# Performance work log

Hardware: AMD Instinct MI355X
Metric: run time of the kernel (lower is better)

Reference implementation:

```python
import jax, jax.numpy as jnp
import numpy as np


def setup_inputs() -> dict:
    key = jax.random.key(0)
    ks = jax.random.split(key, 4)
    B, H, W, C = 4, 64, 64, 64
    d = C // 8
    s = 0.05
    return {
        "x": jax.random.normal(ks[0], (B, H, W, C), dtype=jnp.float32),
        "Wq": jax.random.normal(ks[1], (C, d), dtype=jnp.float32) * s,
        "bq": jnp.zeros((d,), dtype=jnp.float32),
        "Wk": jax.random.normal(ks[2], (C, d), dtype=jnp.float32) * s,
        "bk": jnp.zeros((d,), dtype=jnp.float32),
        "Wv": jax.random.normal(ks[3], (C, C), dtype=jnp.float32) * s,
        "bv": jnp.zeros((C,), dtype=jnp.float32),
        "gamma": jnp.zeros((1,), dtype=jnp.float32),
    }


def reference(x, Wq, bq, Wk, bk, Wv, bv, gamma):
    B, H, W, C = x.shape
    N = H * W
    xt = x.reshape(B, N, C)  # tokens = flattened spatial positions
    # 1x1 convs == per-token matmuls
    q = xt @ Wq + bq          # [B, N, C//8]
    k = xt @ Wk + bk          # [B, N, C//8]
    v = xt @ Wv + bv          # [B, N, C]
    # unscaled QK^T softmax (SAGAN uses no 1/sqrt(d) scaling)
    attn = jax.nn.softmax(jnp.einsum('bnd,bmd->bnm', q, k), axis=-1)  # [B, N, N]
    out = jnp.einsum('bnm,bmc->bnc', attn, v).reshape(B, H, W, C)
    return gamma * out + x
```

## Files before the change

kernel.cpp:

```cpp
#include <hip/hip_runtime.h>
#include <hip/hip_bf16.h>


typedef __attribute__((ext_vector_type(4))) float f32x4;
typedef __attribute__((ext_vector_type(8))) short short8;

#define LOG2E 1.44269504088896340736f

#if __has_builtin(__builtin_amdgcn_exp2f)
#define EXP2(x) __builtin_amdgcn_exp2f(x)
#else
#define EXP2(x) __builtin_exp2f(x)
#endif

__device__ __forceinline__ unsigned short f2bf(float f) {
    __hip_bfloat16 h = __float2bfloat16(f);
    union { __hip_bfloat16 h; unsigned short u; } cv;
    cv.h = h;
    return cv.u;
}

__device__ __forceinline__ float bf2f(unsigned short u) {
    union { unsigned int i; float f; } cv;
    cv.i = ((unsigned int)u) << 16;
    return cv.f;
}

__global__ __launch_bounds__(256) void sagan_proj_kernel(
    const float* __restrict__ x,
    const float* __restrict__ Wq, const float* __restrict__ bq,
    const float* __restrict__ Wk, const float* __restrict__ bk,
    const float* __restrict__ Wv, const float* __restrict__ bv,
    unsigned short* __restrict__ Qb, unsigned short* __restrict__ Kb,
    unsigned char* __restrict__ V8, unsigned short* __restrict__ zp)
{
    __shared__ float xs[32][68];
    const int tid = threadIdx.x;
    const int blk = blockIdx.x;
    const int tglob0 = blk << 5;
    const int b  = tglob0 >> 12;
    const int nb = tglob0 & 4095;

    if (blk == 0 && tid < 8) zp[tid] = 0;

    {
        const int t = tid >> 3, q8 = tid & 7;
        const float* src = x + (size_t)(tglob0 + t) * 64 + q8 * 8;
        *(f32x4*)&xs[t][q8 * 8]     = *(const f32x4*)(src);
        *(f32x4*)&xs[t][q8 * 8 + 4] = *(const f32x4*)(src + 4);
    }
    __syncthreads();

    {
        const int c  = tid & 63;
        const int tg = tid >> 6;
        float wcol[64];
        #pragma unroll
        for (int cc = 0; cc < 64; ++cc) wcol[cc] = Wv[cc * 64 + c];
        const float bvc = bv[c];
        float vacc[8];
        #pragma unroll
        for (int j = 0; j < 8; ++j) {
            const int tok = tg * 8 + j;
            float acc = bvc;
            #pragma unroll
            for (int c4 = 0; c4 < 16; ++c4) {
                f32x4 xv = *(const f32x4*)&xs[tok][c4 * 4];
                acc += xv[0] * wcol[c4 * 4 + 0] + xv[1] * wcol[c4 * 4 + 1]
                     + xv[2] * wcol[c4 * 4 + 2] + xv[3] * wcol[c4 * 4 + 3];
            }
            vacc[j] = acc;
        }
        int i0 = __builtin_amdgcn_cvt_pk_fp8_f32(vacc[0], vacc[1], 0, false);
        i0     = __builtin_amdgcn_cvt_pk_fp8_f32(vacc[2], vacc[3], i0, true);
        int i1 = __builtin_amdgcn_cvt_pk_fp8_f32(vacc[4], vacc[5], 0, false);
        i1     = __builtin_amdgcn_cvt_pk_fp8_f32(vacc[6], vacc[7], i1, true);
        unsigned char* dst = V8 + ((size_t)((b * 128 + (nb >> 5)) * 64 + c)) * 32
                                + tg * 8;
        *(uint2*)dst = make_uint2((unsigned int)i0, (unsigned int)i1);
    }

    {
        const int tok = tid >> 3;
        const int dd  = tid & 7;
        float q0 = bq[dd];
        float k0 = bk[dd];
        #pragma unroll
        for (int cc = 0; cc < 64; ++cc) {
            const float xv = xs[tok][cc];
            q0 += xv * Wq[cc * 8 + dd];
            k0 += xv * Wk[cc * 8 + dd];
        }
        const size_t toff = (size_t)(tglob0 + tok) * 8 + dd;
        Qb[toff] = f2bf(q0 * LOG2E);
        Kb[toff] = f2bf(k0);
    }
}


#define QTILE(KA0, KA1, QF, LL, A0, A1, A2, A3, VF0, VF1, VF2, VF3) do {      \
    const f32x4 zc = {0.f, 0.f, 0.f, 0.f};                                    \
    f32x4 s0 = __builtin_amdgcn_mfma_f32_16x16x32_bf16(KA0, QF, zc, 0, 0, 0); \
    f32x4 s1 = __builtin_amdgcn_mfma_f32_16x16x32_bf16(KA1, QF, zc, 0, 0, 0); \
    float p[8];                                                               \
    _Pragma("unroll")                                                         \
    for (int r = 0; r < 4; ++r) {                                             \
        p[r]     = EXP2(s0[r]);                                               \
        p[4 + r] = EXP2(s1[r]);                                               \
    }                                                                         \
    LL += ((p[0] + p[1]) + (p[2] + p[3])) + ((p[4] + p[5]) + (p[6] + p[7]));  \
    union { int i[2]; long l; } pa;                                           \
    pa.i[0] = __builtin_amdgcn_cvt_pk_fp8_f32(p[0], p[1], 0, false);          \
    pa.i[0] = __builtin_amdgcn_cvt_pk_fp8_f32(p[2], p[3], pa.i[0], true);     \
    pa.i[1] = __builtin_amdgcn_cvt_pk_fp8_f32(p[4], p[5], 0, false);          \
    pa.i[1] = __builtin_amdgcn_cvt_pk_fp8_f32(p[6], p[7], pa.i[1], true);     \
    A0 = __builtin_amdgcn_mfma_f32_16x16x32_fp8_fp8(pa.l, VF0, A0, 0, 0, 0);  \
    A1 = __builtin_amdgcn_mfma_f32_16x16x32_fp8_fp8(pa.l, VF1, A1, 0, 0, 0);  \
    A2 = __builtin_amdgcn_mfma_f32_16x16x32_fp8_fp8(pa.l, VF2, A2, 0, 0, 0);  \
    A3 = __builtin_amdgcn_mfma_f32_16x16x32_fp8_fp8(pa.l, VF3, A3, 0, 0, 0);  \
} while (0)

__global__ __launch_bounds__(512, 4) void sagan_flash_kernel(
    const unsigned short* __restrict__ Qb, const unsigned short* __restrict__ Kb,
    const unsigned char* __restrict__ V8, const unsigned short* __restrict__ zp,
    const float* __restrict__ x, const float* __restrict__ gamma_p,
    float* __restrict__ out)
{
    __shared__ unsigned short sacc[8][32][72];
    __shared__ float sl[8][32];

    const int tid  = threadIdx.x;
    const int lane = tid & 63;
    const int w    = tid >> 6;
    const int g    = lane >> 4;
    const int ql   = lane & 15;
    const int blk  = blockIdx.x;
    const int b    = blk >> 7;
    const int qbase = (blk & 127) << 5;

    const unsigned short* Kbase = Kb + (size_t)b * (4096 * 8);

    const short8 zfrag = {0, 0, 0, 0, 0, 0, 0, 0};
    short8 qf0, qf1;
    {
        short8 a = *(const short8*)(Qb + (size_t)(b * 4096 + qbase + ql) * 8);
        short8 c = *(const short8*)(Qb + (size_t)(b * 4096 + qbase + 16 + ql) * 8);
        qf0 = (g == 0) ? a : zfrag;
        qf1 = (g == 0) ? c : zfrag;
    }

    const int kt0 = w << 9;

    const unsigned short* kp0;
    int kstep;
    if (g == 0) {
        const int kperm = ((ql >> 2) << 3) | (ql & 3);
        kp0 = Kbase + (size_t)(kt0 + kperm) * 8;
        kstep = 256;
    } else {
        kp0 = zp; kstep = 0;
    }

    const unsigned char* vp = V8 + (size_t)(b * 128 + w * 16) * 2048
                                 + ql * 32 + g * 8;

    f32x4 acc00 = {0.f,0.f,0.f,0.f}, acc01 = acc00, acc02 = acc00, acc03 = acc00;
    f32x4 acc10 = acc00, acc11 = acc00, acc12 = acc00, acc13 = acc00;
    float l0 = 0.f, l1 = 0.f;

    #pragma unroll 1
    for (int it = 0; it < 16; ++it) {
        const short8 ka0 = *(const short8*)kp0;
        const short8 ka1 = *(const short8*)(kp0 + 32);
        kp0 += kstep;
        const long vf0 = *(const long*)(vp);
        const long vf1 = *(const long*)(vp + 512);
        const long vf2 = *(const long*)(vp + 1024);
        const long vf3 = *(const long*)(vp + 1536);
        vp += 2048;

        __builtin_amdgcn_s_setprio(1);
        QTILE(ka0, ka1, qf0, l0, acc00, acc01, acc02, acc03,
              vf0, vf1, vf2, vf3);
        QTILE(ka0, ka1, qf1, l1, acc10, acc11, acc12, acc13,
              vf0, vf1, vf2, vf3);
        __builtin_amdgcn_s_setprio(0);
    }

    l0 += __shfl_xor(l0, 16); l0 += __shfl_xor(l0, 32);
    l1 += __shfl_xor(l1, 16); l1 += __shfl_xor(l1, 32);

    #pragma unroll
    for (int r = 0; r < 4; ++r) {
        const int row = (g << 2) | r;
        unsigned short* d0 = &sacc[w][row][0];
        d0[ql] = f2bf(acc00[r]); d0[16 + ql] = f2bf(acc01[r]);
        d0[32 + ql] = f2bf(acc02[r]); d0[48 + ql] = f2bf(acc03[r]);
        unsigned short* d1 = &sacc[w][16 + row][0];
        d1[ql] = f2bf(acc10[r]); d1[16 + ql] = f2bf(acc11[r]);
        d1[32 + ql] = f2bf(acc12[r]); d1[48 + ql] = f2bf(acc13[r]);
    }
    if (g == 0) {
        sl[w][ql] = l0; sl[w][16 + ql] = l1;
    }
    __syncthreads();

    {
        const int row = tid >> 4;
        const int c0  = tid & 15;
        float L = 0.f, O0 = 0.f, O1 = 0.f, O2 = 0.f, O3 = 0.f;
        #pragma unroll
        for (int ww = 0; ww < 8; ++ww) {
            L += sl[ww][row];
            const unsigned short* s = &sacc[ww][row][0];
            O0 += bf2f(s[c0]);      O1 += bf2f(s[c0 + 16]);
            O2 += bf2f(s[c0 + 32]); O3 += bf2f(s[c0 + 48]);
        }
        const float Li = 1.0f / L;
        const float gm = gamma_p[0];
        const size_t rowoff = ((size_t)(b * 4096 + qbase + row)) * 64;
        out[rowoff + c0]      = gm * (O0 * Li) + x[rowoff + c0];
        out[rowoff + c0 + 16] = gm * (O1 * Li) + x[rowoff + c0 + 16];
        out[rowoff + c0 + 32] = gm * (O2 * Li) + x[rowoff + c0 + 32];
        out[rowoff + c0 + 48] = gm * (O3 * Li) + x[rowoff + c0 + 48];
    }
}

extern "C" void kernel_launch(void* const* d_in, const int* in_sizes, int n_in,
                              void* d_out, int out_size, void* d_ws, size_t ws_size,
                              hipStream_t stream) {
    const float* x  = (const float*)d_in[0];
    const float* Wq = (const float*)d_in[1];
    const float* bq = (const float*)d_in[2];
    const float* Wk = (const float*)d_in[3];
    const float* bk = (const float*)d_in[4];
    const float* Wv = (const float*)d_in[5];
    const float* bv = (const float*)d_in[6];
    const float* gm = (const float*)d_in[7];
    float* out = (float*)d_out;

    unsigned short* Qb = (unsigned short*)d_ws;
    unsigned short* Kb = Qb + 131072;
    unsigned char*  V8 = (unsigned char*)(Kb + 131072);
    unsigned short* zp = (unsigned short*)(V8 + 1048576);

    hipLaunchKernelGGL(sagan_proj_kernel, dim3(512), dim3(256), 0, stream,
                       x, Wq, bq, Wk, bk, Wv, bv, Qb, Kb, V8, zp);
    hipLaunchKernelGGL(sagan_flash_kernel, dim3(512), dim3(512), 0, stream,
                       Qb, Kb, V8, zp, x, gm, out);
}
```

Baseline: 28.95 us.

## Use FP8 Q/K scores and widen flash blocks to 64 queries with 16 waves

Q and K are now stored as FP8 instead of bf16, and the score MFMA becomes an fp8×fp8 16x16x32 instruction. The flash kernel moves from 512-thread, 32-query blocks to 1024-thread, 64-query blocks over 256 blocks. Each wave handles 256 keys for four query tiles, which reuses the K and V fragments across more queries. The projection kernel computes two q/k outputs per thread with float2 weight loads. In exchange, Q/K lose precision in the logits, the LDS partial buffer grows to about 148KB (one block per CU), and the cross-wave reduction now covers 16 waves.

Result: slower. 31.56 us (+9.0%).

```diff
diff --git a/kernel.cpp b/kernel.cpp
--- a/kernel.cpp
+++ b/kernel.cpp
@@ -3,7 +3,6 @@
 
 
 typedef __attribute__((ext_vector_type(4))) float f32x4;
-typedef __attribute__((ext_vector_type(8))) short short8;
 
 #define LOG2E 1.44269504088896340736f
 
@@ -31,8 +30,8 @@
     const float* __restrict__ Wq, const float* __restrict__ bq,
     const float* __restrict__ Wk, const float* __restrict__ bk,
     const float* __restrict__ Wv, const float* __restrict__ bv,
-    unsigned short* __restrict__ Qb, unsigned short* __restrict__ Kb,
-    unsigned char* __restrict__ V8, unsigned short* __restrict__ zp)
+    unsigned char* __restrict__ Q8, unsigned char* __restrict__ K8,
+    unsigned char* __restrict__ V8, unsigned char* __restrict__ zp)
 {
     __shared__ float xs[32][68];
     const int tid = threadIdx.x;
@@ -41,13 +40,13 @@
     const int b  = tglob0 >> 12;
     const int nb = tglob0 & 4095;
 
-    if (blk == 0 && tid < 8) zp[tid] = 0;
-
-    {
-        const int t = tid >> 3, q8 = tid & 7;
-        const float* src = x + (size_t)(tglob0 + t) * 64 + q8 * 8;
-        *(f32x4*)&xs[t][q8 * 8]     = *(const f32x4*)(src);
-        *(f32x4*)&xs[t][q8 * 8 + 4] = *(const f32x4*)(src + 4);
+    if (blk == 0 && tid < 16) zp[tid] = 0;
+
+    {
+        const int t = tid >> 3, q8i = tid & 7;
+        const float* src = x + (size_t)(tglob0 + t) * 64 + q8i * 8;
+        *(f32x4*)&xs[t][q8i * 8]     = *(const f32x4*)(src);
+        *(f32x4*)&xs[t][q8i * 8 + 4] = *(const f32x4*)(src + 4);
     }
     __syncthreads();
 
@@ -80,28 +79,32 @@
         *(uint2*)dst = make_uint2((unsigned int)i0, (unsigned int)i1);
     }
 
-    {
-        const int tok = tid >> 3;
-        const int dd  = tid & 7;
-        float q0 = bq[dd];
-        float k0 = bk[dd];
+    if (tid < 128) {
+        const int tok = tid >> 2;
+        const int dp  = (tid & 3) * 2;
+        float q0 = bq[dp], q1 = bq[dp + 1];
+        float k0 = bk[dp], k1 = bk[dp + 1];
         #pragma unroll
         for (int cc = 0; cc < 64; ++cc) {
             const float xv = xs[tok][cc];
-            q0 += xv * Wq[cc * 8 + dd];
-            k0 += xv * Wk[cc * 8 + dd];
+            const float2 wq = *(const float2*)&Wq[cc * 8 + dp];
+            const float2 wk = *(const float2*)&Wk[cc * 8 + dp];
+            q0 += xv * wq.x; q1 += xv * wq.y;
+            k0 += xv * wk.x; k1 += xv * wk.y;
         }
-        const size_t toff = (size_t)(tglob0 + tok) * 8 + dd;
-        Qb[toff] = f2bf(q0 * LOG2E);
-        Kb[toff] = f2bf(k0);
+        const size_t toff = (size_t)(tglob0 + tok) * 8 + dp;
+        const int qi = __builtin_amdgcn_cvt_pk_fp8_f32(q0 * LOG2E, q1 * LOG2E, 0, false);
+        const int ki = __builtin_amdgcn_cvt_pk_fp8_f32(k0, k1, 0, false);
+        *(unsigned short*)(Q8 + toff) = (unsigned short)(qi & 0xFFFF);
+        *(unsigned short*)(K8 + toff) = (unsigned short)(ki & 0xFFFF);
     }
 }
 
 
 #define QTILE(KA0, KA1, QF, LL, A0, A1, A2, A3, VF0, VF1, VF2, VF3) do {      \
     const f32x4 zc = {0.f, 0.f, 0.f, 0.f};                                    \
-    f32x4 s0 = __builtin_amdgcn_mfma_f32_16x16x32_bf16(KA0, QF, zc, 0, 0, 0); \
-    f32x4 s1 = __builtin_amdgcn_mfma_f32_16x16x32_bf16(KA1, QF, zc, 0, 0, 0); \
+    f32x4 s0 = __builtin_amdgcn_mfma_f32_16x16x32_fp8_fp8(KA0, QF, zc, 0,0,0);\
+    f32x4 s1 = __builtin_amdgcn_mfma_f32_16x16x32_fp8_fp8(KA1, QF, zc, 0,0,0);\
     float p[8];                                                               \
     _Pragma("unroll")                                                         \
     for (int r = 0; r < 4; ++r) {                                             \
@@ -120,14 +123,14 @@
     A3 = __builtin_amdgcn_mfma_f32_16x16x32_fp8_fp8(pa.l, VF3, A3, 0, 0, 0);  \
 } while (0)
 
-__global__ __launch_bounds__(512, 4) void sagan_flash_kernel(
-    const unsigned short* __restrict__ Qb, const unsigned short* __restrict__ Kb,
-    const unsigned char* __restrict__ V8, const unsigned short* __restrict__ zp,
+__global__ __launch_bounds__(1024, 4) void sagan_flash_kernel(
+    const unsigned char* __restrict__ Q8, const unsigned char* __restrict__ K8,
+    const unsigned char* __restrict__ V8, const unsigned char* __restrict__ zp,
     const float* __restrict__ x, const float* __restrict__ gamma_p,
     float* __restrict__ out)
 {
-    __shared__ unsigned short sacc[8][32][72];
-    __shared__ float sl[8][32];
+    __shared__ unsigned short sacc[16][64][72];
+    __shared__ float sl[16][64];
 
     const int tid  = threadIdx.x;
     const int lane = tid & 63;
@@ -135,23 +138,24 @@
     const int g    = lane >> 4;
     const int ql   = lane & 15;
     const int blk  = blockIdx.x;
-    const int b    = blk >> 7;
-    const int qbase = (blk & 127) << 5;
-
-    const unsigned short* Kbase = Kb + (size_t)b * (4096 * 8);
-
-    const short8 zfrag = {0, 0, 0, 0, 0, 0, 0, 0};
-    short8 qf0, qf1;
-    {
-        short8 a = *(const short8*)(Qb + (size_t)(b * 4096 + qbase + ql) * 8);
-        short8 c = *(const short8*)(Qb + (size_t)(b * 4096 + qbase + 16 + ql) * 8);
-        qf0 = (g == 0) ? a : zfrag;
-        qf1 = (g == 0) ? c : zfrag;
-    }
-
-    const int kt0 = w << 9;
-
-    const unsigned short* kp0;
+    const int b    = blk >> 6;
+    const int qbase = (blk & 63) << 6;
+
+    const unsigned char* Kbase = K8 + (size_t)b * (4096 * 8);
+    const unsigned char* Qbase = Q8 + (size_t)b * (4096 * 8);
+
+    long qf0, qf1, qf2, qf3;
+    {
+        const unsigned char* qp = Qbase + (size_t)(qbase + ql) * 8;
+        qf0 = (g == 0) ? *(const long*)(qp)       : 0L;
+        qf1 = (g == 0) ? *(const long*)(qp + 128) : 0L;
+        qf2 = (g == 0) ? *(const long*)(qp + 256) : 0L;
+        qf3 = (g == 0) ? *(const long*)(qp + 384) : 0L;
+    }
+
+    const int kt0 = w << 8;
+
+    const unsigned char* kp0;
     int kstep;
     if (g == 0) {
         const int kperm = ((ql >> 2) << 3) | (ql & 3);
@@ -161,17 +165,19 @@
         kp0 = zp; kstep = 0;
     }
 
-    const unsigned char* vp = V8 + (size_t)(b * 128 + w * 16) * 2048
+    const unsigned char* vp = V8 + (size_t)(b * 128 + w * 8) * 2048
                                  + ql * 32 + g * 8;
 
     f32x4 acc00 = {0.f,0.f,0.f,0.f}, acc01 = acc00, acc02 = acc00, acc03 = acc00;
     f32x4 acc10 = acc00, acc11 = acc00, acc12 = acc00, acc13 = acc00;
-    float l0 = 0.f, l1 = 0.f;
+    f32x4 acc20 = acc00, acc21 = acc00, acc22 = acc00, acc23 = acc00;
+    f32x4 acc30 = acc00, acc31 = acc00, acc32 = acc00, acc33 = acc00;
+    float l0 = 0.f, l1 = 0.f, l2 = 0.f, l3 = 0.f;
 
     #pragma unroll 1
-    for (int it = 0; it < 16; ++it) {
-        const short8 ka0 = *(const short8*)kp0;
-        const short8 ka1 = *(const short8*)(kp0 + 32);
+    for (int it = 0; it < 8; ++it) {
+        const long ka0 = *(const long*)kp0;
+        const long ka1 = *(const long*)(kp0 + 32);
         kp0 += kstep;
         const long vf0 = *(const long*)(vp);
         const long vf1 = *(const long*)(vp + 512);
@@ -180,15 +186,17 @@
         vp += 2048;
 
         __builtin_amdgcn_s_setprio(1);
-        QTILE(ka0, ka1, qf0, l0, acc00, acc01, acc02, acc03,
-              vf0, vf1, vf2, vf3);
-        QTILE(ka0, ka1, qf1, l1, acc10, acc11, acc12, acc13,
-              vf0, vf1, vf2, vf3);
+        QTILE(ka0, ka1, qf0, l0, acc00, acc01, acc02, acc03, vf0, vf1, vf2, vf3);
+        QTILE(ka0, ka1, qf1, l1, acc10, acc11, acc12, acc13, vf0, vf1, vf2, vf3);
+        QTILE(ka0, ka1, qf2, l2, acc20, acc21, acc22, acc23, vf0, vf1, vf2, vf3);
+        QTILE(ka0, ka1, qf3, l3, acc30, acc31, acc32, acc33, vf0, vf1, vf2, vf3);
         __builtin_amdgcn_s_setprio(0);
     }
 
     l0 += __shfl_xor(l0, 16); l0 += __shfl_xor(l0, 32);
     l1 += __shfl_xor(l1, 16); l1 += __shfl_xor(l1, 32);
+    l2 += __shfl_xor(l2, 16); l2 += __shfl_xor(l2, 32);
+    l3 += __shfl_xor(l3, 16); l3 += __shfl_xor(l3, 32);
 
     #pragma unroll
     for (int r = 0; r < 4; ++r) {
@@ -199,9 +207,16 @@
         unsigned short* d1 = &sacc[w][16 + row][0];
         d1[ql] = f2bf(acc10[r]); d1[16 + ql] = f2bf(acc11[r]);
         d1[32 + ql] = f2bf(acc12[r]); d1[48 + ql] = f2bf(acc13[r]);
+        unsigned short* d2 = &sacc[w][32 + row][0];
+        d2[ql] = f2bf(acc20[r]); d2[16 + ql] = f2bf(acc21[r]);
+        d2[32 + ql] = f2bf(acc22[r]); d2[48 + ql] = f2bf(acc23[r]);
+        unsigned short* d3 = &sacc[w][48 + row][0];
+        d3[ql] = f2bf(acc30[r]); d3[16 + ql] = f2bf(acc31[r]);
+        d3[32 + ql] = f2bf(acc32[r]); d3[48 + ql] = f2bf(acc33[r]);
     }
     if (g == 0) {
         sl[w][ql] = l0; sl[w][16 + ql] = l1;
+        sl[w][32 + ql] = l2; sl[w][48 + ql] = l3;
     }
     __syncthreads();
 
@@ -210,7 +225,7 @@
         const int c0  = tid & 15;
         float L = 0.f, O0 = 0.f, O1 = 0.f, O2 = 0.f, O3 = 0.f;
         #pragma unroll
-        for (int ww = 0; ww < 8; ++ww) {
+        for (int ww = 0; ww < 16; ++ww) {
             L += sl[ww][row];
             const unsigned short* s = &sacc[ww][row][0];
             O0 += bf2f(s[c0]);      O1 += bf2f(s[c0 + 16]);
@@ -239,13 +254,13 @@
     const float* gm = (const float*)d_in[7];
     float* out = (float*)d_out;
 
-    unsigned short* Qb = (unsigned short*)d_ws;
-    unsigned short* Kb = Qb + 131072;
-    unsigned char*  V8 = (unsigned char*)(Kb + 131072);
-    unsigned short* zp = (unsigned short*)(V8 + 1048576);
+    unsigned char* Q8 = (unsigned char*)d_ws;
+    unsigned char* K8 = Q8 + 131072;
+    unsigned char* V8 = K8 + 131072;
+    unsigned char* zp = V8 + 1048576;
 
     hipLaunchKernelGGL(sagan_proj_kernel, dim3(512), dim3(256), 0, stream,
-                       x, Wq, bq, Wk, bk, Wv, bv, Qb, Kb, V8, zp);
-    hipLaunchKernelGGL(sagan_flash_kernel, dim3(512), dim3(512), 0, stream,
-                       Qb, Kb, V8, zp, x, gm, out);
-}
+                       x, Wq, bq, Wk, bk, Wv, bv, Q8, K8, V8, zp);
+    hipLaunchKernelGGL(sagan_flash_kernel, dim3(256), dim3(1024), 0, stream,
+                       Q8, K8, V8, zp, x, gm, out);
+}
```
